# Performance work log

Measured on AMD Instinct MI355X. Metric: run time of the kernel, lower is better.

Reference implementation:

```python
import jax, jax.numpy as jnp
import numpy as np

BLOCK_SIZE = 64
WINDOW_SIZE = 512
TOPK_BLOCKS = 16
NEG = -1e30


def setup_inputs() -> dict:
    key = jax.random.key(0)
    ks = jax.random.split(key, 6)
    B, T, D = 4, 8192, 256
    return {
        "queries": jax.random.normal(ks[0], (B, T, D), jnp.float32),
        "keys": jax.random.normal(ks[1], (B, T, D), jnp.float32),
        "values": jax.random.normal(ks[2], (B, T, D), jnp.float32),
        "gate_cmp": jax.random.uniform(ks[3], (B, T), jnp.float32),
        "gate_slc": jax.random.uniform(ks[4], (B, T), jnp.float32),
        "gate_swa": jax.random.uniform(ks[5], (B, T), jnp.float32),
    }


def _compress(x, bs):
    # mean-pool tokens into blocks of size bs (pad tail with zeros like F.pad)
    B, T, D = x.shape
    n_blocks = -(-T // bs)
    pad = n_blocks * bs - T
    if pad > 0:
        x = jnp.pad(x, ((0, 0), (0, pad), (0, 0)))
    return x.reshape(B, n_blocks, bs, D).mean(axis=2)  # [B, n_blocks, D]


def _selective(queries, comp_K, comp_V, gate):
    B, T, D = queries.shape
    nb = comp_K.shape[1]
    scale = D ** -0.5
    scores = jnp.einsum("btd,bnd->btn", queries, comp_K) * scale  # [B,T,nb]
    block_ids = jnp.arange(T) // BLOCK_SIZE                       # query's block
    allowed = jnp.arange(nb)[None, :] <= block_ids[:, None]       # no future blocks
    scores = jnp.where(allowed[None], scores, NEG)
    probs = jax.nn.softmax(scores, axis=-1)
    k = min(TOPK_BLOCKS, nb)
    topk_vals, topk_inds = jax.lax.top_k(probs, k)                # [B,T,k]
    gathered = jax.vmap(lambda cv, idx: cv[idx])(comp_V, topk_inds)  # [B,T,k,D]
    sel = jnp.einsum("btk,btkd->btd", topk_vals, gathered)
    return sel * gate[..., None]


def _sliding(queries, keys, values, gate):
    # block-banded sliding-window attention: each query attends to the last
    # WINDOW_SIZE tokens (inclusive of itself), computed per query-block of
    # size W over a 2W key window [block_start - W, block_end).
    B, T, D = queries.shape
    W = WINDOW_SIZE
    n = T // W
    scale = D ** -0.5
    k_pad = jnp.pad(keys, ((0, 0), (W, 0), (0, 0)))   # [B, T+W, D]
    v_pad = jnp.pad(values, ((0, 0), (W, 0), (0, 0)))
    idx = jnp.arange(n)[:, None] * W + jnp.arange(2 * W)[None, :]  # [n, 2W]
    k_win = k_pad[:, idx]                              # [B, n, 2W, D]
    v_win = v_pad[:, idx]
    q_blk = queries.reshape(B, n, W, D)
    scores = jnp.einsum("bnwd,bncd->bnwc", q_blk, k_win) * scale  # [B,n,W,2W]
    r = jnp.arange(W)[:, None]       # row within block
    c = jnp.arange(2 * W)[None, :]   # col within window
    base = (c <= r + W) & (c >= r + 1)                        # [W, 2W] band
    pos_ok = (jnp.arange(n)[:, None, None] * W + c[None] - W) >= 0  # [n,1,2W]
    mask = base[None] & pos_ok                                 # [n, W, 2W]
    scores = jnp.where(mask[None], scores, NEG)
    attn = jax.nn.softmax(scores, axis=-1)
    out = jnp.einsum("bnwc,bncd->bnwd", attn, v_win).reshape(B, T, D)
    return out * gate[..., None]


def reference(queries, keys, values, gate_cmp, gate_slc, gate_swa):
    D = queries.shape[-1]
    scale = D ** -0.5
    comp_K = _compress(keys, BLOCK_SIZE)
    comp_V = _compress(values, BLOCK_SIZE)
    # compressed branch (note: no causal mask, faithful to the source)
    raw = jnp.einsum("btd,bnd->btn", queries, comp_K) * scale
    comp_out = jnp.einsum("btn,bnd->btd", jax.nn.softmax(raw, axis=-1), comp_V)
    comp_out = comp_out * gate_cmp[..., None]
    sel_out = _selective(queries, comp_K, comp_V, gate_slc)
    slide_out = _sliding(queries, keys, values, gate_swa)
    return comp_out + sel_out + slide_out
```

## Files before the change

kernel.cpp:

```cpp
#include <hip/hip_runtime.h>
#include <hip/hip_bf16.h>

#define Tlen 8192
#define Dd 256
#define NBc 128

typedef __attribute__((ext_vector_type(4))) float f32x4;
typedef __attribute__((ext_vector_type(16))) float f32x16;
typedef __attribute__((ext_vector_type(8))) short bf16x8;

__device__ __forceinline__ unsigned short f2bf(float f){
  unsigned u = __builtin_bit_cast(unsigned, f);
  u += 0x7fffu + ((u >> 16) & 1u);
  return (unsigned short)(u >> 16);
}
__device__ __forceinline__ f32x4 mfma16(bf16x8 a, bf16x8 b, f32x4 c){
  return __builtin_amdgcn_mfma_f32_16x16x32_bf16(a, b, c, 0, 0, 0);
}
__device__ __forceinline__ f32x16 mfma32(bf16x8 a, bf16x8 b, f32x16 c){
  return __builtin_amdgcn_mfma_f32_32x32x16_bf16(a, b, c, 0, 0, 0);
}
__device__ __forceinline__ unsigned pkbf(float a, float b){
  unsigned r; asm("v_cvt_pk_bf16_f32 %0, %1, %2" : "=v"(r) : "v"(a), "v"(b)); return r;
}
__device__ __forceinline__ void bar(){
  asm volatile("" ::: "memory");
  __builtin_amdgcn_s_barrier();
  asm volatile("" ::: "memory");
}
__device__ __forceinline__ bf16x8 pack8(f32x4 a0, f32x4 a1){
  bf16x8 o;
  o[0]=(short)f2bf(a0[0]); o[1]=(short)f2bf(a0[1]); o[2]=(short)f2bf(a0[2]); o[3]=(short)f2bf(a0[3]);
  o[4]=(short)f2bf(a1[0]); o[5]=(short)f2bf(a1[1]); o[6]=(short)f2bf(a1[2]); o[7]=(short)f2bf(a1[3]);
  return o;
}
#define GLL16(g, l) __builtin_amdgcn_global_load_lds( \
    (const __attribute__((address_space(1))) unsigned int*)(const void*)(g), \
    (__attribute__((address_space(3))) unsigned int*)(void*)(l), 16, 0, 0)

template<int C>
__device__ __forceinline__ int dppi(int x){
  return __builtin_amdgcn_update_dpp(x, x, C, 0xF, 0xF, false);
}
template<int C>
__device__ __forceinline__ float dppf(float x){
  return __builtin_bit_cast(float, dppi<C>(__builtin_bit_cast(int, x)));
}
__device__ __forceinline__ float dpp_sum16(float x){
  x += dppf<0x121>(x); x += dppf<0x122>(x); x += dppf<0x124>(x); x += dppf<0x128>(x);
  return x;
}

__device__ __forceinline__ bf16x8 load_qfrag(const float* qrow, int kc, int g){
  f32x4 v0 = *(const f32x4*)(qrow + kc*32 + g*8);
  f32x4 v1 = *(const f32x4*)(qrow + kc*32 + g*8 + 4);
  return pack8(v0, v1);
}

__global__ __launch_bounds__(256) void k_prep(const float* __restrict__ K, const float* __restrict__ V,
    unsigned short* __restrict__ ck, unsigned short* __restrict__ cvt,
    unsigned short* __restrict__ Vswz, unsigned short* __restrict__ Kswz, int do_k){
  __shared__ unsigned short Lt[64][72];
  int b = blockIdx.x >> 7, blk = blockIdx.x & 127;
  int t = threadIdx.x;
  const float* Kb = K + ((size_t)b*Tlen + (size_t)blk*64)*Dd;
  const float* Vb = V + ((size_t)b*Tlen + (size_t)blk*64)*Dd;
  {
    float sk=0.f, sv=0.f;
    #pragma unroll 8
    for (int i=0;i<64;i++){ sk += Kb[(size_t)i*Dd + t]; sv += Vb[(size_t)i*Dd + t]; }
    ck[((size_t)b*NBc + blk)*Dd + (((t>>3) ^ (blk&7))<<3) + (t&7)] = f2bf(sk*(1.f/64.f));
    cvt[((size_t)b*Dd + t)*NBc + blk] = f2bf(sv*(1.f/64.f));
  }
  if (do_k){
    unsigned short* kd = Kswz + ((size_t)(b*NBc + blk))*16384;
    #pragma unroll
    for (int i=0;i<8;i++){
      int id = i*256 + t, r = id>>5, c = id&31;
      f32x4 a0 = *(const f32x4*)(Kb + (size_t)r*Dd + c*8);
      f32x4 a1 = *(const f32x4*)(Kb + (size_t)r*Dd + c*8 + 4);
      *(bf16x8*)(kd + r*256 + ((c ^ (r&31))*8)) = pack8(a0,a1);
    }
  }
  unsigned short* vd = Vswz + ((size_t)(b*NBc + blk))*16384;
  for (int dt=0; dt<4; ++dt){
    __syncthreads();
    #pragma unroll
    for (int it=0; it<4; ++it){
      int idx = it*256 + t, r = idx>>4, c4 = idx&15;
      f32x4 v = *(const f32x4*)(Vb + (size_t)r*Dd + dt*64 + c4*4);
      #pragma unroll
      for (int ii=0;ii<4;ii++) Lt[c4*4+ii][r] = f2bf(v[ii]);
    }
    __syncthreads();
    int dd = t>>2, ch = t&3, d = dt*64 + dd;
    unsigned short tmp[16];
    #pragma unroll
    for (int u=0;u<16;u++) tmp[u] = Lt[dd][ch*16+u];
    *(bf16x8*)(vd + d*64 + (((ch*2  ) ^ (d&7))*8)) = *(bf16x8*)(tmp);
    *(bf16x8*)(vd + d*64 + (((ch*2+1) ^ (d&7))*8)) = *(bf16x8*)(tmp+8);
  }
}

__global__ __launch_bounds__(512,4) void k_compsel(const float* __restrict__ Q,
    const unsigned short* __restrict__ ck, const unsigned short* __restrict__ cvt,
    const float* __restrict__ gc, const float* __restrict__ gs, float* __restrict__ out){
  __shared__ __align__(16) unsigned short LB[32768];
  int b = blockIdx.x >> 7, tile = blockIdx.x & 127;
  int q0 = tile*64;
  int t = threadIdx.x, w = t >> 6, l = t & 63, g = l >> 4, lr = l & 15;
  int tr = w >> 1;
  int half = w & 1;

  float gcv[2], gsv[2];
  #pragma unroll
  for (int jl=0;jl<2;jl++){
    int qq = q0 + tr*16 + 4*g + half*2 + jl;
    gcv[jl] = gc[(size_t)b*Tlen + qq];
    gsv[jl] = gs[(size_t)b*Tlen + qq];
  }

  bf16x8 qa[8];
  const float* qrow = Q + ((size_t)b*Tlen + q0 + tr*16 + lr)*Dd;
  #pragma unroll
  for (int kc=0;kc<8;kc++) qa[kc] = load_qfrag(qrow, kc, g);

  {
    const unsigned short* src = ck + (size_t)b*NBc*Dd;
    #pragma unroll
    for (int i=0;i<8;i++){
      int idx = i*512 + t;
      GLL16(src + idx*8, &LB[idx*8]);
    }
  }
  asm volatile("s_waitcnt vmcnt(0)" ::: "memory");
  bar();

  f32x4 acc[8];
  #pragma unroll
  for (int nf=0;nf<8;nf++) acc[nf] = f32x4{0.f,0.f,0.f,0.f};
  #pragma unroll
  for (int nf=0;nf<8;nf++){
    int row = nf*16+lr;
    const unsigned short* rbase = &LB[row*256];
    int xk = row & 7;
    #pragma unroll
    for (int kc=0;kc<8;kc++){
      bf16x8 bb = *(const bf16x8*)(rbase + (((kc*4+g) ^ xk)*8));
      acc[nf] = mfma16(qa[kc], bb, acc[nf]);
    }
  }
  #pragma unroll
  for (int nf=0;nf<8;nf++) acc[nf] *= 0.0625f;
  asm volatile("s_waitcnt lgkmcnt(0)" ::: "memory");
  bar();

  bool al[8];
  #pragma unroll
  for (int nf=0;nf<8;nf++) al[nf] = (nf*16+lr) <= tile;

  float e2[8][2];
  #pragma unroll
  for (int nf=0;nf<8;nf++){
    #pragma unroll
    for (int jl=0;jl<2;jl++) e2[nf][jl] = __expf(acc[nf][half*2+jl]);
  }
  float rzc[2], rzs[2];
  {
    float zc2[2]={0.f,0.f}, zs2[2]={0.f,0.f};
    #pragma unroll
    for (int nf=0;nf<8;nf++){
      #pragma unroll
      for (int jl=0;jl<2;jl++){
        zc2[jl] += e2[nf][jl];
        zs2[jl] += al[nf] ? e2[nf][jl] : 0.f;
      }
    }
    #pragma unroll
    for (int jl=0;jl<2;jl++){
      rzc[jl] = 1.f / dpp_sum16(zc2[jl]);
      rzs[jl] = 1.f / dpp_sum16(zs2[jl]);
    }
  }

  float sm2[8][2];
  #pragma unroll
  for (int nf=0;nf<8;nf++){
    #pragma unroll
    for (int jl=0;jl<2;jl++) sm2[nf][jl] = al[nf] ? acc[nf][half*2+jl] : -3e38f;
  }
  unsigned selm[2]={0,0};
  #pragma unroll 1
  for (int it=0; it<16; ++it){
    float bv[2]; int bi[2];
    #pragma unroll
    for (int jl=0;jl<2;jl++){
      float v = sm2[0][jl]; int n = lr;
      #pragma unroll
      for (int nf=1;nf<8;nf++){
        bool tk = sm2[nf][jl] > v;
        v = tk ? sm2[nf][jl] : v;
        n = tk ? nf*16+lr : n;
      }
      bv[jl]=v; bi[jl]=n;
    }
    #define DSTEP(CTRL) \
    _Pragma("unroll") \
    for (int jl=0;jl<2;jl++){ \
      float ov = dppf<CTRL>(bv[jl]); int oi = dppi<CTRL>(bi[jl]); \
      bool tk = (ov>bv[jl]) || (ov==bv[jl] && oi<bi[jl]); \
      bv[jl] = tk ? ov : bv[jl]; bi[jl] = tk ? oi : bi[jl]; \
    }
    DSTEP(0x121) DSTEP(0x122) DSTEP(0x124) DSTEP(0x128)
    #undef DSTEP
    #pragma unroll
    for (int jl=0;jl<2;jl++){
      selm[jl] |= (((bi[jl]&15)==lr) ? (1u<<(bi[jl]>>4)) : 0u);
      #pragma unroll
      for (int nf=0;nf<8;nf++)
        sm2[nf][jl] = (bi[jl] == nf*16+lr) ? -3e38f : sm2[nf][jl];
    }
  }

  unsigned short* Pc = LB;
  #pragma unroll
  for (int nf=0;nf<8;nf++){
    int n = nf*16+lr;
    #pragma unroll
    for (int jl=0;jl<2;jl++){
      float pcm = e2[nf][jl]*rzc[jl];
      float ps  = (al[nf] && ((selm[jl]>>nf)&1u)) ? e2[nf][jl]*rzs[jl] : 0.f;
      Pc[(tr*16 + 4*g + half*2 + jl)*136 + n] = f2bf(gcv[jl]*pcm + gsv[jl]*ps);
    }
  }
  __syncthreads();

  int rt = w & 3, cf = (w >> 2) * 8;
  bf16x8 pa[4];
  #pragma unroll
  for (int kc=0;kc<4;kc++) pa[kc] = *(const bf16x8*)(&Pc[(rt*16+lr)*136 + kc*32 + g*8]);
  f32x4 po[8];
  #pragma unroll
  for (int i=0;i<8;i++) po[i]=f32x4{0.f,0.f,0.f,0.f};
  const unsigned short* cvb = cvt + (size_t)b*Dd*NBc;
  #pragma unroll
  for (int i2=0;i2<8;i2++){
    int nf2 = cf + i2;
    #pragma unroll
    for (int kc=0;kc<4;kc++){
      bf16x8 vb = *(const bf16x8*)(cvb + (size_t)(nf2*16+lr)*NBc + kc*32 + g*8);
      po[i2] = mfma16(pa[kc], vb, po[i2]);
    }
  }
  #pragma unroll
  for (int i2=0;i2<8;i2++){
    #pragma unroll
    for (int j=0;j<4;j++){
      out[((size_t)b*Tlen + q0 + rt*16 + 4*g + j)*Dd + (cf+i2)*16 + lr] = po[i2][j];
    }
  }
}

template<bool KPRE>
__global__ __launch_bounds__(512,2) void k_swa2(const float* __restrict__ Q, const float* __restrict__ Kf,
    const unsigned short* __restrict__ Kswz, const unsigned short* __restrict__ Vswz,
    const float* __restrict__ gw, float* __restrict__ out, int nt){
  __shared__ __align__(16) unsigned short Ks[2][16384];
  __shared__ __align__(16) unsigned short Ps[8192];

  int wg = blockIdx.x;
  int lin = ((nt & 7) == 0) ? ((wg & 7)*(nt >> 3) + (wg >> 3)) : wg;
  int b = lin >> 6, tile = lin & 63;
  int q0 = tile*128;
  int t = threadIdx.x, w = t>>6, l = t&63;
  int lq = l & 31, h = l >> 5;
  int qf = w & 3, kh = w >> 2;

  bf16x8 qb[16];
  {
    const float* qrow = Q + ((size_t)b*Tlen + q0 + qf*32 + lq)*Dd + h*8;
    #pragma unroll
    for (int kst=0;kst<16;kst++){
      f32x4 a0 = *(const f32x4*)(qrow + kst*16);
      f32x4 a1 = *(const f32x4*)(qrow + kst*16 + 4);
      qb[kst] = pack8(a0, a1);
    }
  }

  f32x16 po[4];
  #pragma unroll
  for (int i=0;i<4;i++) po[i] = (f32x16)(0.f);
  float lacc = 0.f;

  int jb0 = tile*2 - 8; if (jb0 < 0) jb0 = 0;
  const int jbmax = tile*2 + 1;
  const size_t bofK = (size_t)b*NBc*16384;

  auto stage = [&](int buf, int jb){
    const unsigned short* ks = Kswz + bofK + (size_t)jb*16384 + t*8;
    #pragma unroll
    for (int i=0;i<4;i++) GLL16(ks + i*4096, &Ks[buf][t*8 + i*4096]);
  };

  int cur = 0;
  if constexpr (KPRE) stage(0, jb0);

  for (int jb = jb0; jb <= jbmax; ++jb){
    if constexpr (KPRE){
      bar();
      if (jb < jbmax){
        stage(cur^1, jb+1);
        asm volatile("s_waitcnt vmcnt(4)" ::: "memory");
      } else {
        asm volatile("s_waitcnt vmcnt(0)" ::: "memory");
      }
      bar();
    } else {
      bar();
      {
        const float* kb = Kf + ((size_t)b*Tlen + (size_t)jb*64)*Dd;
        #pragma unroll
        for (int i=0;i<4;i++){
          int id = i*512 + t, r = id>>5, c = id&31;
          f32x4 a0 = *(const f32x4*)(kb + (size_t)r*Dd + c*8);
          f32x4 a1 = *(const f32x4*)(kb + (size_t)r*Dd + c*8 + 4);
          *(bf16x8*)(&Ks[0][r*256 + ((c ^ (r&31))*8)]) = pack8(a0,a1);
        }
      }
      asm volatile("s_waitcnt vmcnt(0) lgkmcnt(0)" ::: "memory");
      bar();
    }

    f32x16 s = (f32x16)(0.f);
    {
      int rowK = kh*32 + lq;
      const unsigned short* Krow = &Ks[cur][rowK*256];
      int xk = rowK & 31;
      #pragma unroll
      for (int kst=0;kst<16;kst++){
        bf16x8 kf = *(const bf16x8*)(Krow + (((kst*2 + h) ^ xk)*8));
        s = mfma32(kf, qb[kst], s);
      }
    }
    {
      float pv[16];
      int kbase = jb*64 + kh*32 + 4*h;
      int qg = q0 + qf*32 + lq;
      #pragma unroll
      for (int r=0;r<16;r++){
        int k = kbase + (r&3) + 8*(r>>2);
        float e = (k <= qg && k >= qg-511) ? __expf(s[r]*0.0625f) : 0.f;
        lacc += e; pv[r] = e;
      }
      char* Pr = (char*)&Ps[(qf*32+lq)*64];
      int xq = lq & 7;
      #pragma unroll
      for (int rq=0;rq<4;rq++){
        uint2 val;
        val.x = pkbf(pv[4*rq+0], pv[4*rq+1]);
        val.y = pkbf(pv[4*rq+2], pv[4*rq+3]);
        *(uint2*)(Pr + (((kh*4+rq) ^ xq)*16) + h*8) = val;
      }
    }
    asm volatile("s_waitcnt lgkmcnt(0)" ::: "memory");
    bar();
    {
      const unsigned short* Vrow = Vswz + bofK + (size_t)jb*16384 + (size_t)(w*32+lq)*64;
      int xv = lq & 7;
      bf16x8 vf[4];
      #pragma unroll
      for (int k2=0;k2<4;k2++) vf[k2] = *(const bf16x8*)(Vrow + (((k2*2+h) ^ xv)*8));
      #pragma unroll
      for (int k2=0;k2<4;k2++){
        #pragma unroll
        for (int q2=0;q2<4;q2++){
          const char* Pq = (const char*)&Ps[(q2*32+lq)*64];
          bf16x8 pf = *(const bf16x8*)(Pq + (((k2*2+h) ^ xv)*16));
          po[q2] = mfma32(vf[k2], pf, po[q2]);
        }
      }
    }
    if constexpr (KPRE) cur ^= 1;
  }

  bar();
  float* Lp = (float*)Ps;
  lacc += __shfl_xor(lacc, 32);
  if (l < 32) Lp[kh*128 + qf*32 + l] = lacc;
  __syncthreads();
  #pragma unroll
  for (int q2=0;q2<4;q2++){
    int q = q0 + q2*32 + lq;
    float scale = gw[(size_t)b*Tlen + q] / (Lp[q2*32+lq] + Lp[128 + q2*32+lq]);
    #pragma unroll
    for (int rq=0;rq<4;rq++){
      float* op = out + ((size_t)b*Tlen + q)*Dd + w*32 + rq*8 + h*4;
      f32x4 prev = *(f32x4*)op;
      f32x4 add;
      #pragma unroll
      for (int ii=0;ii<4;ii++) add[ii] = prev[ii] + po[q2][4*rq+ii]*scale;
      *(f32x4*)op = add;
    }
  }
}

extern "C" void kernel_launch(void* const* d_in, const int* in_sizes, int n_in,
                              void* d_out, int out_size, void* d_ws, size_t ws_size,
                              hipStream_t stream) {
  const float* Q  = (const float*)d_in[0];
  const float* K  = (const float*)d_in[1];
  const float* V  = (const float*)d_in[2];
  const float* gc = (const float*)d_in[3];
  const float* gs = (const float*)d_in[4];
  const float* gwp= (const float*)d_in[5];
  float* out = (float*)d_out;
  int B = in_sizes[0] / (Tlen*Dd);

  unsigned short* ck  = (unsigned short*)d_ws;
  unsigned short* cvt = ck  + (size_t)B*NBc*Dd;
  unsigned short* Vsw = cvt + (size_t)B*Dd*NBc;
  unsigned short* Ksw = Vsw + (size_t)B*Tlen*Dd;

  size_t need_full = ((size_t)B*((size_t)NBc*Dd + (size_t)Dd*NBc + 2*(size_t)Tlen*Dd))*2;
  bool kpre = ws_size >= need_full;
  int nt = B*64;

  k_prep   <<<dim3(B*128), dim3(256), 0, stream>>>(K, V, ck, cvt, Vsw, Ksw, kpre?1:0);
  k_compsel<<<dim3(B*128), dim3(512), 0, stream>>>(Q, ck, cvt, gc, gs, out);
  if (kpre) k_swa2<true ><<<dim3(nt), dim3(512), 0, stream>>>(Q, K, Ksw, Vsw, gwp, out, nt);
  else      k_swa2<false><<<dim3(nt), dim3(512), 0, stream>>>(Q, K, Ksw, Vsw, gwp, out, nt);
}
```

Baseline: 119.5 us.

## Rewrite sliding-window kernel with 64-query tiles and 16x16 MFMA

The sliding-window attention kernel now handles 64 queries per workgroup instead of 128, which doubles the grid. It switches from 32x32x16 to 16x16x32 bf16 MFMA fragments, halves the P buffer in shared memory, and raises launch bounds to allow 4 workgroups per CU. The K swizzle changes from XOR with row&31 to row&7, applied consistently in prep and in the loads. The goal is better occupancy and load balance and less wasted masked work per tile. In exchange, each key block is reloaded by twice as many workgroups, so K/V traffic rises, and register pressure under the tighter launch bounds could cause spills.

```diff
diff --git a/kernel.cpp b/kernel.cpp
--- a/kernel.cpp
+++ b/kernel.cpp
@@ -16,9 +16,6 @@
 }
 __device__ __forceinline__ f32x4 mfma16(bf16x8 a, bf16x8 b, f32x4 c){
   return __builtin_amdgcn_mfma_f32_16x16x32_bf16(a, b, c, 0, 0, 0);
-}
-__device__ __forceinline__ f32x16 mfma32(bf16x8 a, bf16x8 b, f32x16 c){
-  return __builtin_amdgcn_mfma_f32_32x32x16_bf16(a, b, c, 0, 0, 0);
 }
 __device__ __forceinline__ unsigned pkbf(float a, float b){
   unsigned r; asm("v_cvt_pk_bf16_f32 %0, %1, %2" : "=v"(r) : "v"(a), "v"(b)); return r;
@@ -79,7 +76,7 @@
       int id = i*256 + t, r = id>>5, c = id&31;
       f32x4 a0 = *(const f32x4*)(Kb + (size_t)r*Dd + c*8);
       f32x4 a1 = *(const f32x4*)(Kb + (size_t)r*Dd + c*8 + 4);
-      *(bf16x8*)(kd + r*256 + ((c ^ (r&31))*8)) = pack8(a0,a1);
+      *(bf16x8*)(kd + r*256 + ((c ^ (r&7))*8)) = pack8(a0,a1);
     }
   }
   unsigned short* vd = Vswz + ((size_t)(b*NBc + blk))*16384;
@@ -262,46 +259,40 @@
 }
 
 template<bool KPRE>
-__global__ __launch_bounds__(512,2) void k_swa2(const float* __restrict__ Q, const float* __restrict__ Kf,
+__global__ __launch_bounds__(512,4) void k_swa3(const float* __restrict__ Q, const float* __restrict__ Kf,
     const unsigned short* __restrict__ Kswz, const unsigned short* __restrict__ Vswz,
     const float* __restrict__ gw, float* __restrict__ out, int nt){
   __shared__ __align__(16) unsigned short Ks[2][16384];
-  __shared__ __align__(16) unsigned short Ps[8192];
+  __shared__ __align__(16) unsigned short Ps[4096];
+  __shared__ float Lp[2][64];
 
   int wg = blockIdx.x;
   int lin = ((nt & 7) == 0) ? ((wg & 7)*(nt >> 3) + (wg >> 3)) : wg;
-  int b = lin >> 6, tile = lin & 63;
-  int q0 = tile*128;
-  int t = threadIdx.x, w = t>>6, l = t&63;
-  int lq = l & 31, h = l >> 5;
-  int qf = w & 3, kh = w >> 2;
-
-  bf16x8 qb[16];
-  {
-    const float* qrow = Q + ((size_t)b*Tlen + q0 + qf*32 + lq)*Dd + h*8;
-    #pragma unroll
-    for (int kst=0;kst<16;kst++){
-      f32x4 a0 = *(const f32x4*)(qrow + kst*16);
-      f32x4 a1 = *(const f32x4*)(qrow + kst*16 + 4);
-      qb[kst] = pack8(a0, a1);
-    }
-  }
-
-  f32x16 po[4];
-  #pragma unroll
-  for (int i=0;i<4;i++) po[i] = (f32x16)(0.f);
-  float lacc = 0.f;
-
-  int jb0 = tile*2 - 8; if (jb0 < 0) jb0 = 0;
-  const int jbmax = tile*2 + 1;
-  const size_t bofK = (size_t)b*NBc*16384;
+  int b = lin >> 7, tile = lin & 127;
+  int q0 = tile*64;
+  int t = threadIdx.x, w = t>>6, l = t&63, g = l>>4, lr = l&15;
+  int rg = w & 3;
+  int kh = w >> 2;
+
+  bf16x8 qa[8];
+  const float* qrow = Q + ((size_t)b*Tlen + q0 + rg*16 + lr)*Dd;
+  #pragma unroll
+  for (int kc=0;kc<8;kc++) qa[kc] = load_qfrag(qrow, kc, g);
+
+  f32x4 po[8];
+  #pragma unroll
+  for (int i=0;i<8;i++) po[i]=f32x4{0.f,0.f,0.f,0.f};
+  float zs[4] = {0.f,0.f,0.f,0.f};
+
+  int jb0 = tile - 8; if (jb0 < 0) jb0 = 0;
+  const int jbmax = tile;
+  const size_t bof = (size_t)b*NBc*16384;
 
   auto stage = [&](int buf, int jb){
-    const unsigned short* ks = Kswz + bofK + (size_t)jb*16384 + t*8;
+    const unsigned short* ks = Kswz + bof + (size_t)jb*16384 + t*8;
     #pragma unroll
     for (int i=0;i<4;i++) GLL16(ks + i*4096, &Ks[buf][t*8 + i*4096]);
   };
-
   int cur = 0;
   if constexpr (KPRE) stage(0, jb0);
 
@@ -324,82 +315,94 @@
           int id = i*512 + t, r = id>>5, c = id&31;
           f32x4 a0 = *(const f32x4*)(kb + (size_t)r*Dd + c*8);
           f32x4 a1 = *(const f32x4*)(kb + (size_t)r*Dd + c*8 + 4);
-          *(bf16x8*)(&Ks[0][r*256 + ((c ^ (r&31))*8)]) = pack8(a0,a1);
+          *(bf16x8*)(&Ks[0][r*256 + ((c ^ (r&7))*8)]) = pack8(a0,a1);
         }
       }
       asm volatile("s_waitcnt vmcnt(0) lgkmcnt(0)" ::: "memory");
       bar();
     }
 
-    f32x16 s = (f32x16)(0.f);
-    {
-      int rowK = kh*32 + lq;
-      const unsigned short* Krow = &Ks[cur][rowK*256];
-      int xk = rowK & 31;
-      #pragma unroll
-      for (int kst=0;kst<16;kst++){
-        bf16x8 kf = *(const bf16x8*)(Krow + (((kst*2 + h) ^ xk)*8));
-        s = mfma32(kf, qb[kst], s);
-      }
-    }
-    {
-      float pv[16];
-      int kbase = jb*64 + kh*32 + 4*h;
-      int qg = q0 + qf*32 + lq;
-      #pragma unroll
-      for (int r=0;r<16;r++){
-        int k = kbase + (r&3) + 8*(r>>2);
-        float e = (k <= qg && k >= qg-511) ? __expf(s[r]*0.0625f) : 0.f;
-        lacc += e; pv[r] = e;
-      }
-      char* Pr = (char*)&Ps[(qf*32+lq)*64];
-      int xq = lq & 7;
-      #pragma unroll
-      for (int rq=0;rq<4;rq++){
-        uint2 val;
-        val.x = pkbf(pv[4*rq+0], pv[4*rq+1]);
-        val.y = pkbf(pv[4*rq+2], pv[4*rq+3]);
-        *(uint2*)(Pr + (((kh*4+rq) ^ xq)*16) + h*8) = val;
+    f32x4 acc[2];
+    acc[0]=f32x4{0.f,0.f,0.f,0.f}; acc[1]=f32x4{0.f,0.f,0.f,0.f};
+    #pragma unroll
+    for (int nf=0;nf<2;nf++){
+      int key = kh*32 + nf*16 + lr;
+      const unsigned short* rbase = &Ks[cur][key*256];
+      int xk = key & 7;
+      #pragma unroll
+      for (int kc=0;kc<8;kc++){
+        bf16x8 kf = *(const bf16x8*)(rbase + (((kc*4+g) ^ xk)*8));
+        acc[nf] = mfma16(qa[kc], kf, acc[nf]);
+      }
+    }
+    #pragma unroll
+    for (int nf=0;nf<2;nf++){
+      int kloc = kh*32 + nf*16 + lr;
+      int kglob = jb*64 + kloc;
+      int kchunk = kloc >> 3;
+      #pragma unroll
+      for (int j=0;j<4;j++){
+        int qloc = rg*16 + 4*g + j;
+        int qg2 = q0 + qloc;
+        float e = (kglob <= qg2 && kglob >= qg2-511) ? __expf(acc[nf][j]*0.0625f) : 0.f;
+        zs[j] += e;
+        Ps[qloc*64 + ((kchunk ^ (qloc&7))<<3) + (lr&7)] = f2bf(e);
       }
     }
     asm volatile("s_waitcnt lgkmcnt(0)" ::: "memory");
     bar();
+
     {
-      const unsigned short* Vrow = Vswz + bofK + (size_t)jb*16384 + (size_t)(w*32+lq)*64;
-      int xv = lq & 7;
-      bf16x8 vf[4];
-      #pragma unroll
-      for (int k2=0;k2<4;k2++) vf[k2] = *(const bf16x8*)(Vrow + (((k2*2+h) ^ xv)*8));
-      #pragma unroll
-      for (int k2=0;k2<4;k2++){
+      bf16x8 vf[2][2];
+      #pragma unroll
+      for (int nf2=0;nf2<2;nf2++){
+        int d = w*32 + nf2*16 + lr;
+        const unsigned short* vrow = Vswz + bof + (size_t)jb*16384 + (size_t)d*64;
+        int xv = d & 7;
         #pragma unroll
-        for (int q2=0;q2<4;q2++){
-          const char* Pq = (const char*)&Ps[(q2*32+lq)*64];
-          bf16x8 pf = *(const bf16x8*)(Pq + (((k2*2+h) ^ xv)*16));
-          po[q2] = mfma32(vf[k2], pf, po[q2]);
+        for (int k2=0;k2<2;k2++)
+          vf[nf2][k2] = *(const bf16x8*)(vrow + (((k2*4+g) ^ xv)*8));
+      }
+      #pragma unroll
+      for (int rg2=0;rg2<4;rg2++){
+        int qloc = rg2*16 + lr;
+        int xq = qloc & 7;
+        bf16x8 pa0 = *(const bf16x8*)(&Ps[qloc*64 + (((0*4+g) ^ xq)<<3)]);
+        bf16x8 pa1 = *(const bf16x8*)(&Ps[qloc*64 + (((1*4+g) ^ xq)<<3)]);
+        #pragma unroll
+        for (int nf2=0;nf2<2;nf2++){
+          po[rg2*2+nf2] = mfma16(pa0, vf[nf2][0], po[rg2*2+nf2]);
+          po[rg2*2+nf2] = mfma16(pa1, vf[nf2][1], po[rg2*2+nf2]);
         }
       }
     }
     if constexpr (KPRE) cur ^= 1;
   }
 
-  bar();
-  float* Lp = (float*)Ps;
-  lacc += __shfl_xor(lacc, 32);
-  if (l < 32) Lp[kh*128 + qf*32 + l] = lacc;
+  #pragma unroll
+  for (int j=0;j<4;j++) zs[j] = dpp_sum16(zs[j]);
+  if (lr == 0){
+    #pragma unroll
+    for (int j=0;j<4;j++) Lp[kh][rg*16 + 4*g + j] = zs[j];
+  }
   __syncthreads();
-  #pragma unroll
-  for (int q2=0;q2<4;q2++){
-    int q = q0 + q2*32 + lq;
-    float scale = gw[(size_t)b*Tlen + q] / (Lp[q2*32+lq] + Lp[128 + q2*32+lq]);
-    #pragma unroll
-    for (int rq=0;rq<4;rq++){
-      float* op = out + ((size_t)b*Tlen + q)*Dd + w*32 + rq*8 + h*4;
-      f32x4 prev = *(f32x4*)op;
-      f32x4 add;
-      #pragma unroll
-      for (int ii=0;ii<4;ii++) add[ii] = prev[ii] + po[q2][4*rq+ii]*scale;
-      *(f32x4*)op = add;
+
+  #pragma unroll
+  for (int rg2=0;rg2<4;rg2++){
+    float scl[4];
+    #pragma unroll
+    for (int j=0;j<4;j++){
+      int qloc = rg2*16 + 4*g + j;
+      int q = q0 + qloc;
+      scl[j] = gw[(size_t)b*Tlen + q] / (Lp[0][qloc] + Lp[1][qloc]);
+    }
+    #pragma unroll
+    for (int nf2=0;nf2<2;nf2++){
+      #pragma unroll
+      for (int j=0;j<4;j++){
+        size_t o = ((size_t)b*Tlen + q0 + rg2*16 + 4*g + j)*Dd + w*32 + nf2*16 + lr;
+        out[o] += po[rg2*2+nf2][j] * scl[j];
+      }
     }
   }
 }
@@ -423,10 +426,10 @@
 
   size_t need_full = ((size_t)B*((size_t)NBc*Dd + (size_t)Dd*NBc + 2*(size_t)Tlen*Dd))*2;
   bool kpre = ws_size >= need_full;
-  int nt = B*64;
+  int nt = B*128;
 
   k_prep   <<<dim3(B*128), dim3(256), 0, stream>>>(K, V, ck, cvt, Vsw, Ksw, kpre?1:0);
   k_compsel<<<dim3(B*128), dim3(512), 0, stream>>>(Q, ck, cvt, gc, gs, out);
-  if (kpre) k_swa2<true ><<<dim3(nt), dim3(512), 0, stream>>>(Q, K, Ksw, Vsw, gwp, out, nt);
-  else      k_swa2<false><<<dim3(nt), dim3(512), 0, stream>>>(Q, K, Ksw, Vsw, gwp, out, nt);
-}
+  if (kpre) k_swa3<true ><<<dim3(nt), dim3(512), 0, stream>>>(Q, K, Ksw, Vsw, gwp, out, nt);
+  else      k_swa3<false><<<dim3(nt), dim3(512), 0, stream>>>(Q, K, Ksw, Vsw, gwp, out, nt);
+}
```

Result: faster. 115.1 us (-3.7%).
